# Kernel tuning notes

Measured on AMD Instinct MI355X. Metric: run time of the kernel, lower is better.

## Reference

```python
import jax, jax.numpy as jnp
import numpy as np

T, B = 256, 64
NTOKEN, NINP, NHID = 256, 64, 4096


def setup_inputs() -> dict:
    key = jax.random.key(0)
    k1, k2, k3, k4, k5, k6, k7 = jax.random.split(key, 7)
    tokens = jax.random.randint(k1, (T, B), 0, NTOKEN)            # [T, B] byte ids
    seq_len = jax.random.randint(k2, (B,), 1, T + 1)              # per-sample valid length in [1, T]
    s_in = 1.0 / np.sqrt(NINP)
    s_h = 1.0 / np.sqrt(NHID)
    emb_table = jax.random.normal(k3, (NTOKEN, NINP), jnp.float32)
    w_ih = jax.random.normal(k4, (4 * NHID, NINP), jnp.float32) * s_in
    w_hh = jax.random.normal(k5, (4 * NHID, NHID), jnp.float32) * s_h
    b_ih = jax.random.normal(k6, (4 * NHID,), jnp.float32) * s_h
    b_hh = jax.random.normal(k7, (4 * NHID,), jnp.float32) * s_h
    return {"tokens": tokens, "seq_len": seq_len, "emb_table": emb_table,
            "w_ih": w_ih, "w_hh": w_hh, "b_ih": b_ih, "b_hh": b_hh}


def reference(tokens, seq_len, emb_table, w_ih, w_hh, b_ih, b_hh):
    # Embedding lookup for all timesteps (dropout p=0.0 -> identity).
    emb = emb_table[tokens]                                   # [T, B, ninp]
    # Precompute input projections for every step (batched GEMM).
    x_proj = jnp.einsum('tbi,gi->tbg', emb, w_ih) + b_ih + b_hh  # [T, B, 4H]
    H = w_hh.shape[1]
    h0 = jnp.zeros((tokens.shape[1], H), x_proj.dtype)
    c0 = jnp.zeros_like(h0)
    feat0 = jnp.zeros_like(h0)

    def step(carry, inp):
        h, c, feat = carry
        xp, t = inp
        gates = xp + h @ w_hh.T                               # [B, 4H]
        i_g, f_g, g_g, o_g = jnp.split(gates, 4, axis=-1)     # torch gate order i,f,g,o
        c = jax.nn.sigmoid(f_g) * c + jax.nn.sigmoid(i_g) * jnp.tanh(g_g)
        h = jax.nn.sigmoid(o_g) * jnp.tanh(c)
        # get_valid_outs: at step t>0, keep previous feature once t >= seq_len.
        valid = (t < seq_len) | (t == 0)                      # [B]
        feat = jnp.where(valid[:, None], c, feat)
        return (h, c, feat), None

    (_, _, feat), _ = jax.lax.scan(step, (h0, c0, feat0),
                                   (x_proj, jnp.arange(x_proj.shape[0])))
    return feat                                               # [B, nhid]
```

## Files before the change

### kernel.cpp

```cpp
#include <hip/hip_runtime.h>
#include <hip/hip_bf16.h>

#define TSTEPS 256
#define BATCH  64
#define NINP   64
#define NHID   4096
#define NGATE  (4 * NHID)
#define KDIM   (NINP + NHID)
#define NCHUNK (KDIM / 32)
#define NGRP   (NGATE / 16)

typedef __bf16 bf16x8 __attribute__((ext_vector_type(8)));
typedef float  f32x4  __attribute__((ext_vector_type(4)));
typedef unsigned short ushort_t;

__device__ __forceinline__ ushort_t f2b(float v) {
    __hip_bfloat16 h = __float2bfloat16(v);
    return *reinterpret_cast<ushort_t*>(&h);
}
__device__ __forceinline__ float sigf(float x) { return 1.f / (1.f + expf(-x)); }


__global__ void k_convert(const float* __restrict__ w_ih, const float* __restrict__ w_hh,
                          const float* __restrict__ b_ih, const float* __restrict__ b_hh,
                          ushort_t* __restrict__ Wp, float* __restrict__ bias) {
    const int grp = blockIdx.x;
    for (int i = threadIdx.x; i < 16 * KDIM; i += 256) {
        int r = i / KDIM;
        int k = i - r * KDIM;
        int g = grp * 16 + r;
        float v = (k < NINP) ? w_ih[(size_t)g * NINP + k]
                             : w_hh[(size_t)g * NHID + (k - NINP)];
        int c = k >> 5, q = (k >> 3) & 3, e = k & 7;
        Wp[((size_t)grp * NCHUNK + c) * 512 + (q * 16 + r) * 8 + e] = f2b(v);
    }
    if (threadIdx.x < 16) {
        int g = grp * 16 + threadIdx.x;
        bias[g] = b_ih[g] + b_hh[g];
    }
}

__global__ void k_init(const int* __restrict__ tokens, const float* __restrict__ emb,
                       ushort_t* __restrict__ A0, float* __restrict__ cbuf) {
    int idx = blockIdx.x * 256 + threadIdx.x;
    if (idx < BATCH * KDIM) {
        int b = idx / KDIM, k = idx - b * KDIM;
        float v = (k < NINP) ? emb[tokens[b] * NINP + k] : 0.f;
        int c = k >> 5, q = (k >> 3) & 3, e = k & 7;
        A0[((size_t)(b >> 4) * NCHUNK + c) * 512 + (q * 16 + (b & 15)) * 8 + e] = f2b(v);
    }
    if (idx < BATCH * NHID) cbuf[idx] = 0.f;
}

__global__ __launch_bounds__(512)
void k_step(int t, const ushort_t* __restrict__ Wp, const float* __restrict__ bias,
            const ushort_t* __restrict__ Ac, ushort_t* __restrict__ An,
            float* __restrict__ cbuf, float* __restrict__ out,
            const int* __restrict__ tokens, const int* __restrict__ seq_len,
            const float* __restrict__ emb) {
    const int tid  = threadIdx.x;
    const int wave = tid >> 6;
    const int lane = tid & 63;
    const int bx   = blockIdx.x;
    const int j0   = bx * 16;

    __shared__ float sbuf[BATCH][66];

    for (int i = tid; i < BATCH * 66; i += 512)
        (&sbuf[0][0])[i] = 0.f;

    if (bx == 0 && (t + 1) < TSTEPS) {
        for (int i = tid; i < BATCH * NINP; i += 512) {
            int b = i >> 6, k = i & 63;
            int tok = tokens[(t + 1) * BATCH + b];
            float v = emb[tok * NINP + k];
            int c = k >> 5, q = (k >> 3) & 3, e = k & 7;
            An[((size_t)(b >> 4) * NCHUNK + c) * 512 + (q * 16 + (b & 15)) * 8 + e] = f2b(v);
        }
    }
    __syncthreads();

    const int cstart = wave * 16 + (wave < 2 ? wave : 2);
    const int cend   = cstart + (wave < 2 ? 17 : 16);

    const ushort_t* pw0 = Wp + ((size_t)(0 * 256 + bx) * NCHUNK) * 512 + lane * 8;
    const ushort_t* pw1 = Wp + ((size_t)(1 * 256 + bx) * NCHUNK) * 512 + lane * 8;
    const ushort_t* pw2 = Wp + ((size_t)(2 * 256 + bx) * NCHUNK) * 512 + lane * 8;
    const ushort_t* pw3 = Wp + ((size_t)(3 * 256 + bx) * NCHUNK) * 512 + lane * 8;
    const ushort_t* pa0 = Ac + ((size_t)0 * NCHUNK) * 512 + lane * 8;
    const ushort_t* pa1 = Ac + ((size_t)1 * NCHUNK) * 512 + lane * 8;
    const ushort_t* pa2 = Ac + ((size_t)2 * NCHUNK) * 512 + lane * 8;
    const ushort_t* pa3 = Ac + ((size_t)3 * NCHUNK) * 512 + lane * 8;

    f32x4 acc[4][4];
    #pragma unroll
    for (int rt = 0; rt < 4; ++rt)
        #pragma unroll
        for (int gt = 0; gt < 4; ++gt)
            acc[rt][gt] = (f32x4){0.f, 0.f, 0.f, 0.f};

    #define LOADF(dstW, dstA, c)                                              \
        do {                                                                  \
            size_t off = (size_t)(c) * 512;                                   \
            dstW[0] = *reinterpret_cast<const bf16x8*>(pw0 + off);            \
            dstW[1] = *reinterpret_cast<const bf16x8*>(pw1 + off);            \
            dstW[2] = *reinterpret_cast<const bf16x8*>(pw2 + off);            \
            dstW[3] = *reinterpret_cast<const bf16x8*>(pw3 + off);            \
            dstA[0] = *reinterpret_cast<const bf16x8*>(pa0 + off);            \
            dstA[1] = *reinterpret_cast<const bf16x8*>(pa1 + off);            \
            dstA[2] = *reinterpret_cast<const bf16x8*>(pa2 + off);            \
            dstA[3] = *reinterpret_cast<const bf16x8*>(pa3 + off);            \
        } while (0)

    bf16x8 curW[4], curA[4], nxtW[4], nxtA[4];
    LOADF(curW, curA, cstart);

    for (int c = cstart; c < cend - 1; ++c) {
        LOADF(nxtW, nxtA, c + 1);
        #pragma unroll
        for (int rt = 0; rt < 4; ++rt)
            #pragma unroll
            for (int gt = 0; gt < 4; ++gt)
                acc[rt][gt] = __builtin_amdgcn_mfma_f32_16x16x32_bf16(
                    curA[rt], curW[gt], acc[rt][gt], 0, 0, 0);
        #pragma unroll
        for (int z = 0; z < 4; ++z) { curW[z] = nxtW[z]; curA[z] = nxtA[z]; }
    }
    #pragma unroll
    for (int rt = 0; rt < 4; ++rt)
        #pragma unroll
        for (int gt = 0; gt < 4; ++gt)
            acc[rt][gt] = __builtin_amdgcn_mfma_f32_16x16x32_bf16(
                curA[rt], curW[gt], acc[rt][gt], 0, 0, 0);
    #undef LOADF

    {
        const int n = lane & 15, q = lane >> 4;
        #pragma unroll
        for (int rt = 0; rt < 4; ++rt)
            #pragma unroll
            for (int gt = 0; gt < 4; ++gt)
                #pragma unroll
                for (int r = 0; r < 4; ++r)
                    atomicAdd(&sbuf[rt * 16 + q * 4 + r][gt * 16 + n], acc[rt][gt][r]);
    }
    __syncthreads();

    {
        const int b  = lane;
        const int sl = seq_len[b];
        const bool valid = (t < sl) || (t == 0);
        #pragma unroll
        for (int jj = 0; jj < 2; ++jj) {
            int jl = wave + jj * 8;
            int j  = j0 + jl;
            float ig = sbuf[b][ 0 + jl] + bias[          j];
            float fg = sbuf[b][16 + jl] + bias[    NHID + j];
            float gg = sbuf[b][32 + jl] + bias[2 * NHID + j];
            float og = sbuf[b][48 + jl] + bias[3 * NHID + j];
            int cidx = b * NHID + j;
            float cold = cbuf[cidx];
            float cn = sigf(fg) * cold + sigf(ig) * tanhf(gg);
            float hn = sigf(og) * tanhf(cn);
            cbuf[cidx] = cn;
            if (valid) out[cidx] = cn;
            int kk = NINP + j;
            int c = kk >> 5, q = (kk >> 3) & 3, e = kk & 7;
            An[((size_t)(b >> 4) * NCHUNK + c) * 512 + (q * 16 + (b & 15)) * 8 + e] = f2b(hn);
        }
    }
}

extern "C" void kernel_launch(void* const* d_in, const int* in_sizes, int n_in,
                              void* d_out, int out_size, void* d_ws, size_t ws_size,
                              hipStream_t stream) {
    const int*   tokens  = (const int*)d_in[0];
    const int*   seq_len = (const int*)d_in[1];
    const float* emb     = (const float*)d_in[2];
    const float* w_ih    = (const float*)d_in[3];
    const float* w_hh    = (const float*)d_in[4];
    const float* b_ih    = (const float*)d_in[5];
    const float* b_hh    = (const float*)d_in[6];
    float* out = (float*)d_out;

    char* ws = (char*)d_ws;
    const size_t W_BYTES    = (size_t)NGRP * NCHUNK * 512 * 2;
    const size_t BIAS_BYTES = (size_t)NGATE * 4;
    const size_t C_BYTES    = (size_t)BATCH * NHID * 4;
    const size_t A_BYTES    = (size_t)4 * NCHUNK * 512 * 2;

    ushort_t* Wp   = (ushort_t*)ws;
    float*    bias = (float*)(ws + W_BYTES);
    float*    cbuf = (float*)(ws + W_BYTES + BIAS_BYTES);
    ushort_t* A0   = (ushort_t*)(ws + W_BYTES + BIAS_BYTES + C_BYTES);
    ushort_t* A1   = (ushort_t*)(ws + W_BYTES + BIAS_BYTES + C_BYTES + A_BYTES);

    k_convert<<<NGRP, 256, 0, stream>>>(w_ih, w_hh, b_ih, b_hh, Wp, bias);

    int init_elems = BATCH * KDIM;
    k_init<<<(init_elems + 255) / 256, 256, 0, stream>>>(tokens, emb, A0, cbuf);

    for (int t = 0; t < TSTEPS; ++t) {
        ushort_t* Acur  = (t & 1) ? A1 : A0;
        ushort_t* Anext = (t & 1) ? A0 : A1;
        k_step<<<256, 512, 0, stream>>>(t, Wp, bias, Acur, Anext, cbuf, out,
                                        tokens, seq_len, emb);
    }
}
```

Baseline: 17.19 ms.

## Fuse per-timestep launches into a persistent kernel with a grid barrier

Replaces the 256 separate per-step launches with one persistent kernel of 256 blocks. The blocks synchronise between timesteps through an atomic counter barrier in global memory. Cell state now lives in shared memory instead of a global buffer, biases are held in registers, and the output is written only once, at the last valid step of each sequence. The embedding load for the next step is spread across all blocks, and the weight/activation prefetch is reworked into a two-stage ping-pong. This removes launch gaps and some global traffic. In exchange it relies on all blocks being co-resident, and the spin barrier carries a guard that could silently break out of the wait.

```diff
diff --git a/kernel.cpp b/kernel.cpp
--- a/kernel.cpp
+++ b/kernel.cpp
@@ -9,6 +9,7 @@
 #define KDIM   (NINP + NHID)
 #define NCHUNK (KDIM / 32)
 #define NGRP   (NGATE / 16)
+#define NBLK   256
 
 typedef __bf16 bf16x8 __attribute__((ext_vector_type(8)));
 typedef float  f32x4  __attribute__((ext_vector_type(4)));
@@ -41,7 +42,7 @@
 }
 
 __global__ void k_init(const int* __restrict__ tokens, const float* __restrict__ emb,
-                       ushort_t* __restrict__ A0, float* __restrict__ cbuf) {
+                       ushort_t* __restrict__ A0) {
     int idx = blockIdx.x * 256 + threadIdx.x;
     if (idx < BATCH * KDIM) {
         int b = idx / KDIM, k = idx - b * KDIM;
@@ -49,15 +50,14 @@
         int c = k >> 5, q = (k >> 3) & 3, e = k & 7;
         A0[((size_t)(b >> 4) * NCHUNK + c) * 512 + (q * 16 + (b & 15)) * 8 + e] = f2b(v);
     }
-    if (idx < BATCH * NHID) cbuf[idx] = 0.f;
-}
-
-__global__ __launch_bounds__(512)
-void k_step(int t, const ushort_t* __restrict__ Wp, const float* __restrict__ bias,
-            const ushort_t* __restrict__ Ac, ushort_t* __restrict__ An,
-            float* __restrict__ cbuf, float* __restrict__ out,
-            const int* __restrict__ tokens, const int* __restrict__ seq_len,
-            const float* __restrict__ emb) {
+}
+
+__global__ __launch_bounds__(512, 2)
+void k_persist(const ushort_t* __restrict__ Wp, const float* __restrict__ bias,
+               ushort_t* __restrict__ A0, ushort_t* __restrict__ A1,
+               float* __restrict__ out,
+               const int* __restrict__ tokens, const int* __restrict__ seq_len,
+               const float* __restrict__ emb, unsigned* __restrict__ bar) {
     const int tid  = threadIdx.x;
     const int wave = tid >> 6;
     const int lane = tid & 63;
@@ -65,110 +65,139 @@
     const int j0   = bx * 16;
 
     __shared__ float sbuf[BATCH][66];
-
-    for (int i = tid; i < BATCH * 66; i += 512)
-        (&sbuf[0][0])[i] = 0.f;
-
-    if (bx == 0 && (t + 1) < TSTEPS) {
-        for (int i = tid; i < BATCH * NINP; i += 512) {
-            int b = i >> 6, k = i & 63;
-            int tok = tokens[(t + 1) * BATCH + b];
-            float v = emb[tok * NINP + k];
-            int c = k >> 5, q = (k >> 3) & 3, e = k & 7;
-            An[((size_t)(b >> 4) * NCHUNK + c) * 512 + (q * 16 + (b & 15)) * 8 + e] = f2b(v);
-        }
-    }
-    __syncthreads();
+    __shared__ float creg[BATCH][17];
+
+    for (int i2 = tid; i2 < BATCH * 17; i2 += 512) (&creg[0][0])[i2] = 0.f;
+
+    const int sl = seq_len[lane];
+    float bi[4][2];
+    #pragma unroll
+    for (int g = 0; g < 4; ++g)
+        #pragma unroll
+        for (int jj = 0; jj < 2; ++jj)
+            bi[g][jj] = bias[g * NHID + j0 + wave + jj * 8];
 
     const int cstart = wave * 16 + (wave < 2 ? wave : 2);
-    const int cend   = cstart + (wave < 2 ? 17 : 16);
+    const int NC     = (wave < 2 ? 17 : 16);
 
     const ushort_t* pw0 = Wp + ((size_t)(0 * 256 + bx) * NCHUNK) * 512 + lane * 8;
     const ushort_t* pw1 = Wp + ((size_t)(1 * 256 + bx) * NCHUNK) * 512 + lane * 8;
     const ushort_t* pw2 = Wp + ((size_t)(2 * 256 + bx) * NCHUNK) * 512 + lane * 8;
     const ushort_t* pw3 = Wp + ((size_t)(3 * 256 + bx) * NCHUNK) * 512 + lane * 8;
-    const ushort_t* pa0 = Ac + ((size_t)0 * NCHUNK) * 512 + lane * 8;
-    const ushort_t* pa1 = Ac + ((size_t)1 * NCHUNK) * 512 + lane * 8;
-    const ushort_t* pa2 = Ac + ((size_t)2 * NCHUNK) * 512 + lane * 8;
-    const ushort_t* pa3 = Ac + ((size_t)3 * NCHUNK) * 512 + lane * 8;
-
-    f32x4 acc[4][4];
-    #pragma unroll
-    for (int rt = 0; rt < 4; ++rt)
-        #pragma unroll
-        for (int gt = 0; gt < 4; ++gt)
-            acc[rt][gt] = (f32x4){0.f, 0.f, 0.f, 0.f};
-
-    #define LOADF(dstW, dstA, c)                                              \
-        do {                                                                  \
-            size_t off = (size_t)(c) * 512;                                   \
-            dstW[0] = *reinterpret_cast<const bf16x8*>(pw0 + off);            \
-            dstW[1] = *reinterpret_cast<const bf16x8*>(pw1 + off);            \
-            dstW[2] = *reinterpret_cast<const bf16x8*>(pw2 + off);            \
-            dstW[3] = *reinterpret_cast<const bf16x8*>(pw3 + off);            \
-            dstA[0] = *reinterpret_cast<const bf16x8*>(pa0 + off);            \
-            dstA[1] = *reinterpret_cast<const bf16x8*>(pa1 + off);            \
-            dstA[2] = *reinterpret_cast<const bf16x8*>(pa2 + off);            \
-            dstA[3] = *reinterpret_cast<const bf16x8*>(pa3 + off);            \
-        } while (0)
-
-    bf16x8 curW[4], curA[4], nxtW[4], nxtA[4];
-    LOADF(curW, curA, cstart);
-
-    for (int c = cstart; c < cend - 1; ++c) {
-        LOADF(nxtW, nxtA, c + 1);
+
+    const int eb = bx >> 2;
+    const int ek = (bx & 3) * 16;
+
+    #define LOADF(WD, AD, cc) do {                                        \
+        const size_t _o = (size_t)(cc) * 512;                             \
+        WD[0] = *reinterpret_cast<const bf16x8*>(pw0 + _o);               \
+        WD[1] = *reinterpret_cast<const bf16x8*>(pw1 + _o);               \
+        WD[2] = *reinterpret_cast<const bf16x8*>(pw2 + _o);               \
+        WD[3] = *reinterpret_cast<const bf16x8*>(pw3 + _o);               \
+        AD[0] = *reinterpret_cast<const bf16x8*>(pa0 + _o);               \
+        AD[1] = *reinterpret_cast<const bf16x8*>(pa1 + _o);               \
+        AD[2] = *reinterpret_cast<const bf16x8*>(pa2 + _o);               \
+        AD[3] = *reinterpret_cast<const bf16x8*>(pa3 + _o);               \
+    } while (0)
+
+    #define DOMFMA(WD, AD) do {                                           \
+        _Pragma("unroll")                                                 \
+        for (int _rt = 0; _rt < 4; ++_rt) {                               \
+            _Pragma("unroll")                                             \
+            for (int _gt = 0; _gt < 4; ++_gt)                             \
+                acc[_rt][_gt] = __builtin_amdgcn_mfma_f32_16x16x32_bf16(  \
+                    AD[_rt], WD[_gt], acc[_rt][_gt], 0, 0, 0);            \
+        }                                                                 \
+    } while (0)
+
+    for (int t = 0; t < TSTEPS; ++t) {
+        ushort_t* Ac = (t & 1) ? A1 : A0;
+        ushort_t* An = (t & 1) ? A0 : A1;
+
+        for (int i2 = tid; i2 < BATCH * 66; i2 += 512) (&sbuf[0][0])[i2] = 0.f;
+
+        const ushort_t* pa0 = Ac + (size_t)(0 * NCHUNK) * 512 + lane * 8;
+        const ushort_t* pa1 = Ac + (size_t)(1 * NCHUNK) * 512 + lane * 8;
+        const ushort_t* pa2 = Ac + (size_t)(2 * NCHUNK) * 512 + lane * 8;
+        const ushort_t* pa3 = Ac + (size_t)(3 * NCHUNK) * 512 + lane * 8;
+
+        f32x4 acc[4][4];
         #pragma unroll
         for (int rt = 0; rt < 4; ++rt)
             #pragma unroll
             for (int gt = 0; gt < 4; ++gt)
-                acc[rt][gt] = __builtin_amdgcn_mfma_f32_16x16x32_bf16(
-                    curA[rt], curW[gt], acc[rt][gt], 0, 0, 0);
-        #pragma unroll
-        for (int z = 0; z < 4; ++z) { curW[z] = nxtW[z]; curA[z] = nxtA[z]; }
-    }
-    #pragma unroll
-    for (int rt = 0; rt < 4; ++rt)
-        #pragma unroll
-        for (int gt = 0; gt < 4; ++gt)
-            acc[rt][gt] = __builtin_amdgcn_mfma_f32_16x16x32_bf16(
-                curA[rt], curW[gt], acc[rt][gt], 0, 0, 0);
+                acc[rt][gt] = (f32x4){0.f, 0.f, 0.f, 0.f};
+
+        bf16x8 wA[4], xA[4], wB[4], xB[4];
+        LOADF(wA, xA, cstart);
+        LOADF(wB, xB, cstart + 1);
+        int i = 0;
+        for (; i + 2 < NC; i += 2) {
+            DOMFMA(wA, xA);
+            LOADF(wA, xA, cstart + i + 2);
+            DOMFMA(wB, xB);
+            if (i + 3 < NC) LOADF(wB, xB, cstart + i + 3);
+        }
+        DOMFMA(wA, xA);
+        if ((NC & 1) == 0) DOMFMA(wB, xB);
+
+        __syncthreads();
+        {
+            const int n = lane & 15, q = lane >> 4;
+            #pragma unroll
+            for (int rt = 0; rt < 4; ++rt)
+                #pragma unroll
+                for (int gt = 0; gt < 4; ++gt)
+                    #pragma unroll
+                    for (int r = 0; r < 4; ++r)
+                        atomicAdd(&sbuf[rt * 16 + q * 4 + r][gt * 16 + n], acc[rt][gt][r]);
+        }
+        __syncthreads();
+
+        {
+            const int b = lane;
+            #pragma unroll
+            for (int jj = 0; jj < 2; ++jj) {
+                const int jl = wave + jj * 8;
+                const int j  = j0 + jl;
+                float ig = sbuf[b][ 0 + jl] + bi[0][jj];
+                float fg = sbuf[b][16 + jl] + bi[1][jj];
+                float gg = sbuf[b][32 + jl] + bi[2][jj];
+                float og = sbuf[b][48 + jl] + bi[3][jj];
+                float cold = creg[b][jl];
+                float cn = sigf(fg) * cold + sigf(ig) * tanhf(gg);
+                float hn = sigf(og) * tanhf(cn);
+                creg[b][jl] = cn;
+                if (t == sl - 1) out[b * NHID + j] = cn;
+                const int kk = NINP + j;
+                const int c = kk >> 5, q2 = (kk >> 3) & 3, e = kk & 7;
+                An[((size_t)(b >> 4) * NCHUNK + c) * 512 + (q2 * 16 + (b & 15)) * 8 + e] = f2b(hn);
+            }
+            if (tid < 16 && (t + 1) < TSTEPS) {
+                const int k   = ek + tid;
+                const int tok = tokens[(t + 1) * BATCH + eb];
+                const float v = emb[tok * NINP + k];
+                const int c = k >> 5, q2 = (k >> 3) & 3, e = k & 7;
+                An[((size_t)(eb >> 4) * NCHUNK + c) * 512 + (q2 * 16 + (eb & 15)) * 8 + e] = f2b(v);
+            }
+        }
+
+        __syncthreads();
+        if (tid == 0) {
+            __hip_atomic_fetch_add(bar, 1u, __ATOMIC_RELEASE, __HIP_MEMORY_SCOPE_AGENT);
+            const unsigned tgt = (unsigned)(t + 1) * NBLK;
+            int guard = 0;
+            while (__hip_atomic_load(bar, __ATOMIC_RELAXED, __HIP_MEMORY_SCOPE_AGENT) < tgt) {
+                __builtin_amdgcn_s_sleep(2);
+                if (++guard > (1 << 20)) break;
+            }
+        }
+        __syncthreads();
+        __builtin_amdgcn_fence(__ATOMIC_ACQUIRE, "agent");
+    }
+
     #undef LOADF
-
-    {
-        const int n = lane & 15, q = lane >> 4;
-        #pragma unroll
-        for (int rt = 0; rt < 4; ++rt)
-            #pragma unroll
-            for (int gt = 0; gt < 4; ++gt)
-                #pragma unroll
-                for (int r = 0; r < 4; ++r)
-                    atomicAdd(&sbuf[rt * 16 + q * 4 + r][gt * 16 + n], acc[rt][gt][r]);
-    }
-    __syncthreads();
-
-    {
-        const int b  = lane;
-        const int sl = seq_len[b];
-        const bool valid = (t < sl) || (t == 0);
-        #pragma unroll
-        for (int jj = 0; jj < 2; ++jj) {
-            int jl = wave + jj * 8;
-            int j  = j0 + jl;
-            float ig = sbuf[b][ 0 + jl] + bias[          j];
-            float fg = sbuf[b][16 + jl] + bias[    NHID + j];
-            float gg = sbuf[b][32 + jl] + bias[2 * NHID + j];
-            float og = sbuf[b][48 + jl] + bias[3 * NHID + j];
-            int cidx = b * NHID + j;
-            float cold = cbuf[cidx];
-            float cn = sigf(fg) * cold + sigf(ig) * tanhf(gg);
-            float hn = sigf(og) * tanhf(cn);
-            cbuf[cidx] = cn;
-            if (valid) out[cidx] = cn;
-            int kk = NINP + j;
-            int c = kk >> 5, q = (kk >> 3) & 3, e = kk & 7;
-            An[((size_t)(b >> 4) * NCHUNK + c) * 512 + (q * 16 + (b & 15)) * 8 + e] = f2b(hn);
-        }
-    }
+    #undef DOMFMA
 }
 
 extern "C" void kernel_launch(void* const* d_in, const int* in_sizes, int n_in,
@@ -186,24 +215,22 @@
     char* ws = (char*)d_ws;
     const size_t W_BYTES    = (size_t)NGRP * NCHUNK * 512 * 2;
     const size_t BIAS_BYTES = (size_t)NGATE * 4;
-    const size_t C_BYTES    = (size_t)BATCH * NHID * 4;
+    const size_t BAR_BYTES  = 1024;
     const size_t A_BYTES    = (size_t)4 * NCHUNK * 512 * 2;
 
     ushort_t* Wp   = (ushort_t*)ws;
     float*    bias = (float*)(ws + W_BYTES);
-    float*    cbuf = (float*)(ws + W_BYTES + BIAS_BYTES);
-    ushort_t* A0   = (ushort_t*)(ws + W_BYTES + BIAS_BYTES + C_BYTES);
-    ushort_t* A1   = (ushort_t*)(ws + W_BYTES + BIAS_BYTES + C_BYTES + A_BYTES);
+    unsigned* bar  = (unsigned*)(ws + W_BYTES + BIAS_BYTES);
+    ushort_t* A0   = (ushort_t*)(ws + W_BYTES + BIAS_BYTES + BAR_BYTES);
+    ushort_t* A1   = (ushort_t*)(ws + W_BYTES + BIAS_BYTES + BAR_BYTES + A_BYTES);
+
+    hipMemsetAsync(bar, 0, 8, stream);
 
     k_convert<<<NGRP, 256, 0, stream>>>(w_ih, w_hh, b_ih, b_hh, Wp, bias);
 
     int init_elems = BATCH * KDIM;
-    k_init<<<(init_elems + 255) / 256, 256, 0, stream>>>(tokens, emb, A0, cbuf);
-
-    for (int t = 0; t < TSTEPS; ++t) {
-        ushort_t* Acur  = (t & 1) ? A1 : A0;
-        ushort_t* Anext = (t & 1) ? A0 : A1;
-        k_step<<<256, 512, 0, stream>>>(t, Wp, bias, Acur, Anext, cbuf, out,
-                                        tokens, seq_len, emb);
-    }
-}
+    k_init<<<(init_elems + 255) / 256, 256, 0, stream>>>(tokens, emb, A0);
+
+    k_persist<<<NBLK, 512, 0, stream>>>(Wp, bias, A0, A1, out,
+                                        tokens, seq_len, emb, bar);
+}
```

Measured after the change: 23.69 ms. +37.8%, slower.
